# Performance work log

Hardware: AMD Instinct MI355X
Metric: run time of the kernel (lower is better)

The kernel has to match this reference:

```python
import jax, jax.numpy as jnp
import numpy as np

B, DM, L = 16, 512, 1024
D_INNER, D_STATE, D_CONV, DT_RANK = 1024, 16, 4, 32


def setup_inputs() -> dict:
    key = jax.random.key(0)
    ks = jax.random.split(key, 10)
    x = jax.random.normal(ks[0], (B, DM, L), dtype=jnp.float32)
    W_in = jax.random.normal(ks[1], (DM, 2 * D_INNER), dtype=jnp.float32) * 0.02
    conv_w = jax.random.normal(ks[2], (D_INNER, D_CONV), dtype=jnp.float32) * 0.1
    conv_b = jnp.zeros((D_INNER,), dtype=jnp.float32)
    W_x = jax.random.normal(ks[3], (D_INNER, DT_RANK + 2 * D_STATE), dtype=jnp.float32) * 0.02
    W_dt = jax.random.normal(ks[4], (DT_RANK, D_INNER), dtype=jnp.float32) * (DT_RANK ** -0.5)
    dt = jnp.exp(jax.random.uniform(ks[5], (D_INNER,), dtype=jnp.float32)
                 * (np.log(0.1) - np.log(1e-3)) + np.log(1e-3))
    dt_bias = dt + jnp.log(-jnp.expm1(-dt))  # inverse softplus
    A_log = jnp.log(jnp.tile(jnp.arange(1, D_STATE + 1, dtype=jnp.float32)[None, :], (D_INNER, 1)))
    D_skip = jnp.ones((D_INNER,), dtype=jnp.float32)
    W_out = jax.random.normal(ks[6], (D_INNER, DM), dtype=jnp.float32) * 0.02
    gamma = jnp.ones((DM,), dtype=jnp.float32)
    beta = jnp.zeros((DM,), dtype=jnp.float32)
    return {"x": x, "W_in": W_in, "conv_w": conv_w, "conv_b": conv_b, "W_x": W_x,
            "W_dt": W_dt, "dt_bias": dt_bias, "A_log": A_log, "D_skip": D_skip,
            "W_out": W_out, "gamma": gamma, "beta": beta}


def _mamba(xt, W_in, conv_w, conv_b, W_x, W_dt, dt_bias, A_log, D_skip, W_out):
    # xt: [B, L, DM]
    b, l, _ = xt.shape
    xz = xt @ W_in                                   # [B, L, 2*D_INNER]
    xi, z = jnp.split(xz, 2, axis=-1)                # each [B, L, D_INNER]
    # causal depthwise conv1d, kernel D_CONV
    xp = jnp.pad(xi, ((0, 0), (D_CONV - 1, 0), (0, 0)))
    xc = sum(xp[:, k:k + l, :] * conv_w[None, None, :, k] for k in range(D_CONV))
    xc = jax.nn.silu(xc + conv_b)                    # [B, L, D_INNER]
    proj = xc @ W_x                                  # [B, L, DT_RANK + 2*D_STATE]
    dt_in = proj[..., :DT_RANK]
    Bm = proj[..., DT_RANK:DT_RANK + D_STATE]        # [B, L, D_STATE]
    Cm = proj[..., DT_RANK + D_STATE:]               # [B, L, D_STATE]
    delta = jax.nn.softplus(dt_in @ W_dt + dt_bias)  # [B, L, D_INNER]
    A = -jnp.exp(A_log)                              # [D_INNER, D_STATE]

    def step(h, inp):
        d, bt, ct, u = inp                           # [B,Di], [B,Ds], [B,Ds], [B,Di]
        dA = jnp.exp(d[:, :, None] * A[None])        # [B, Di, Ds]
        h = dA * h + d[:, :, None] * bt[:, None, :] * u[:, :, None]
        y = jnp.einsum('bds,bs->bd', h, ct)
        return h, y

    h0 = jnp.zeros((b, D_INNER, D_STATE), dtype=xt.dtype)
    elems = (jnp.swapaxes(delta, 0, 1), jnp.swapaxes(Bm, 0, 1),
             jnp.swapaxes(Cm, 0, 1), jnp.swapaxes(xc, 0, 1))
    _, ys = jax.lax.scan(step, h0, elems)            # ys: [L, B, D_INNER]
    y = jnp.swapaxes(ys, 0, 1) + xc * D_skip
    y = y * jax.nn.silu(z)
    return y @ W_out                                 # [B, L, DM]


def reference(x, W_in, conv_w, conv_b, W_x, W_dt, dt_bias, A_log, D_skip, W_out, gamma, beta):
    xt = jnp.swapaxes(x, 1, 2)                       # (B, DM, L) -> (B, L, DM)
    xt = xt + _mamba(xt, W_in, conv_w, conv_b, W_x, W_dt, dt_bias, A_log, D_skip, W_out)
    mu = jnp.mean(xt, axis=-1, keepdims=True)
    var = jnp.mean(jnp.square(xt - mu), axis=-1, keepdims=True)
    xt = (xt - mu) * jax.lax.rsqrt(var + 1e-5) * gamma + beta
    return jnp.swapaxes(xt, 1, 2)                    # back to (B, DM, L)
```

## Files before the change

kernel.cpp:

```cpp
#include <hip/hip_runtime.h>
#include <hip/hip_bf16.h>
#include <math.h>

#define B_SZ 16
#define DM 512
#define LSEQ 1024
#define DI 1024
#define DSTATE 16
#define DTR 32
#define MROWS (B_SZ * LSEQ)
#define NC 16
#define SCH (LSEQ / NC)
#define PF 4

typedef __attribute__((ext_vector_type(8))) short bf16x8;
typedef __attribute__((ext_vector_type(4))) float f32x4;

__device__ inline float bfu2f(unsigned short u) {
  union { unsigned int i; float f; } c; c.i = ((unsigned int)u) << 16; return c.f;
}
__device__ inline unsigned short f2bfu(float f) {
  union { float f; unsigned int i; } c; c.f = f;
  unsigned int r = c.i + 0x7fff + ((c.i >> 16) & 1);
  return (unsigned short)(r >> 16);
}
__device__ inline f32x4 splat4(float x) { return (f32x4){x, x, x, x}; }

__device__ inline void gl_lds16(const unsigned short* g, unsigned short* l) {
  __builtin_amdgcn_global_load_lds(
      (const __attribute__((address_space(1))) unsigned int*)g,
      (__attribute__((address_space(3))) unsigned int*)l, 16, 0, 0);
}

__global__ void transpose_x_k(const float* __restrict__ x, unsigned short* __restrict__ xtb) {
  __shared__ float t[32][33];
  int b = blockIdx.z;
  int l0 = blockIdx.x * 32, dm0 = blockIdx.y * 32;
  int tx = threadIdx.x, ty = threadIdx.y;
  for (int i = ty; i < 32; i += 8)
    t[i][tx] = x[((long)b * DM + dm0 + i) * LSEQ + l0 + tx];
  __syncthreads();
  for (int i = ty; i < 32; i += 8) {
    long o = ((long)b * LSEQ + l0 + i) * DM + dm0 + tx;
    xtb[o] = f2bfu(t[tx][i]);
  }
}

__global__ void wtrans_k(const float* __restrict__ W, unsigned short* __restrict__ Wt,
                         int N, int K) {
  __shared__ float t[32][33];
  int n0 = blockIdx.x * 32, k0 = blockIdx.y * 32;
  int tx = threadIdx.x, ty = threadIdx.y;
  for (int i = ty; i < 32; i += 8)
    t[i][tx] = W[(long)(k0 + i) * N + n0 + tx];
  __syncthreads();
  for (int i = ty; i < 32; i += 8)
    Wt[(long)(n0 + i) * K + k0 + tx] = f2bfu(t[tx][i]);
}

template <int BM, int BN, int WMN, int WNN, int EPI>
__global__ __launch_bounds__(256, 4) void gemm_bt(
    const unsigned short* __restrict__ A, const unsigned short* __restrict__ Bt,
    void* __restrict__ outp, void* __restrict__ outp2,
    const unsigned short* __restrict__ res, int N, int K) {
  constexpr int WM = BM / WMN;
  constexpr int WN = BN / WNN;
  constexpr int MR = WM / 16;
  constexpr int NR = WN / 16;
  __shared__ __align__(16) unsigned short As[2][BM * 32];
  __shared__ __align__(16) unsigned short Bs[2][BN * 32];
  const int tid = threadIdx.x;
  const int lane = tid & 63;
  const int w = tid >> 6;
  const int wm = w / WNN, wn = w % WNN;
  const long rowT = (long)blockIdx.y * BM;
  const long colT = (long)blockIdx.x * BN;

  f32x4 acc[MR][NR];
#pragma unroll
  for (int m = 0; m < MR; ++m)
#pragma unroll
    for (int n = 0; n < NR; ++n)
      acc[m][n] = (f32x4){0.f, 0.f, 0.f, 0.f};

  const int mrow = wm * WM + (lane & 15);
  const int ncol = wn * WN + (lane & 15);
  const int k8 = (lane >> 4) * 8;
  const int srow = (lane >> 2);
  const int scol = (lane & 3) * 8;

  auto STAGE = [&](int buf, int k0) {
#pragma unroll
    for (int i = 0; i < BM / 64; ++i) {
      int r = i * 64 + w * 16;
      gl_lds16(A + (rowT + r + srow) * K + k0 + scol, &As[buf][r * 32]);
    }
#pragma unroll
    for (int i = 0; i < BN / 64; ++i) {
      int r = i * 64 + w * 16;
      gl_lds16(Bt + (colT + r + srow) * K + k0 + scol, &Bs[buf][r * 32]);
    }
  };

  STAGE(0, 0);
  __syncthreads();
  int cur = 0;
  const int NT = K / 32;
  for (int kt = 0; kt < NT; ++kt) {
    if (kt + 1 < NT) STAGE(cur ^ 1, (kt + 1) * 32);
    bf16x8 af[MR], bfr[NR];
#pragma unroll
    for (int m = 0; m < MR; ++m)
      af[m] = *(const bf16x8*)(&As[cur][(mrow + m * 16) * 32 + k8]);
#pragma unroll
    for (int n = 0; n < NR; ++n)
      bfr[n] = *(const bf16x8*)(&Bs[cur][(ncol + n * 16) * 32 + k8]);
#pragma unroll
    for (int m = 0; m < MR; ++m)
#pragma unroll
      for (int n = 0; n < NR; ++n)
        acc[m][n] = __builtin_amdgcn_mfma_f32_16x16x32_bf16(af[m], bfr[n], acc[m][n], 0, 0, 0);
    __syncthreads();
    cur ^= 1;
  }

  if (EPI == 3) {
    unsigned short* obase = (colT < DI) ? (unsigned short*)outp : (unsigned short*)outp2;
    const long csub = (colT < DI) ? 0 : DI;
#pragma unroll
    for (int m = 0; m < MR; ++m)
#pragma unroll
      for (int n = 0; n < NR; ++n)
#pragma unroll
        for (int r = 0; r < 4; ++r) {
          long row = rowT + wm * WM + m * 16 + (lane >> 4) * 4 + r;
          long col = colT + wn * WN + n * 16 + (lane & 15) - csub;
          obase[row * DI + col] = f2bfu(acc[m][n][r]);
        }
  } else {
#pragma unroll
    for (int m = 0; m < MR; ++m)
#pragma unroll
      for (int n = 0; n < NR; ++n)
#pragma unroll
        for (int r = 0; r < 4; ++r) {
          long row = rowT + wm * WM + m * 16 + (lane >> 4) * 4 + r;
          long col = colT + wn * WN + n * 16 + (lane & 15);
          float v = acc[m][n][r];
          if (EPI == 0)
            ((float*)outp)[row * N + col] = v;
          else
            ((float*)outp)[row * N + col] = v + bfu2f(res[row * N + col]);
        }
  }
}

template <int BM, int BN, int WMN, int WNN, int EPI>
__global__ __launch_bounds__(512, 4) void gemm_bt8(
    const unsigned short* __restrict__ A, const unsigned short* __restrict__ Bt,
    void* __restrict__ outp, void* __restrict__ outp2,
    const unsigned short* __restrict__ res, int N, int K) {
  constexpr int WM = BM / WMN;
  constexpr int WN = BN / WNN;
  constexpr int MR = WM / 16;
  constexpr int NR = WN / 16;
  __shared__ __align__(16) unsigned short As[2][BM * 32];
  __shared__ __align__(16) unsigned short Bs[2][BN * 32];
  const int tid = threadIdx.x;
  const int lane = tid & 63;
  const int w = tid >> 6;
  const int wm = w / WNN, wn = w % WNN;
  const long rowT = (long)blockIdx.y * BM;
  const long colT = (long)blockIdx.x * BN;

  f32x4 acc[MR][NR];
#pragma unroll
  for (int m = 0; m < MR; ++m)
#pragma unroll
    for (int n = 0; n < NR; ++n)
      acc[m][n] = (f32x4){0.f, 0.f, 0.f, 0.f};

  const int mrow = wm * WM + (lane & 15);
  const int ncol = wn * WN + (lane & 15);
  const int k8 = (lane >> 4) * 8;
  const int srow = (lane >> 2);
  const int scol = (lane & 3) * 8;

  auto STAGE = [&](int buf, int k0) {
#pragma unroll
    for (int i = 0; i < BM / 128; ++i) {
      int r = i * 128 + w * 16;
      gl_lds16(A + (rowT + r + srow) * K + k0 + scol, &As[buf][r * 32]);
    }
#pragma unroll
    for (int i = 0; i < BN / 128; ++i) {
      int r = i * 128 + w * 16;
      gl_lds16(Bt + (colT + r + srow) * K + k0 + scol, &Bs[buf][r * 32]);
    }
  };

  STAGE(0, 0);
  __syncthreads();
  int cur = 0;
  const int NT = K / 32;
  for (int kt = 0; kt < NT; ++kt) {
    if (kt + 1 < NT) STAGE(cur ^ 1, (kt + 1) * 32);
    bf16x8 af[MR], bfr[NR];
#pragma unroll
    for (int m = 0; m < MR; ++m)
      af[m] = *(const bf16x8*)(&As[cur][(mrow + m * 16) * 32 + k8]);
#pragma unroll
    for (int n = 0; n < NR; ++n)
      bfr[n] = *(const bf16x8*)(&Bs[cur][(ncol + n * 16) * 32 + k8]);
#pragma unroll
    for (int m = 0; m < MR; ++m)
#pragma unroll
      for (int n = 0; n < NR; ++n)
        acc[m][n] = __builtin_amdgcn_mfma_f32_16x16x32_bf16(af[m], bfr[n], acc[m][n], 0, 0, 0);
    __syncthreads();
    cur ^= 1;
  }

  if (EPI == 3) {
    unsigned short* obase = (colT < DI) ? (unsigned short*)outp : (unsigned short*)outp2;
    const long csub = (colT < DI) ? 0 : DI;
#pragma unroll
    for (int m = 0; m < MR; ++m)
#pragma unroll
      for (int n = 0; n < NR; ++n)
#pragma unroll
        for (int r = 0; r < 4; ++r) {
          long row = rowT + wm * WM + m * 16 + (lane >> 4) * 4 + r;
          long col = colT + wn * WN + n * 16 + (lane & 15) - csub;
          obase[row * DI + col] = f2bfu(acc[m][n][r]);
        }
  } else {
#pragma unroll
    for (int m = 0; m < MR; ++m)
#pragma unroll
      for (int n = 0; n < NR; ++n)
#pragma unroll
        for (int r = 0; r < 4; ++r) {
          long row = rowT + wm * WM + m * 16 + (lane >> 4) * 4 + r;
          long col = colT + wn * WN + n * 16 + (lane & 15);
          float v = acc[m][n][r];
          if (EPI == 0)
            ((float*)outp)[row * N + col] = v;
          else
            ((float*)outp)[row * N + col] = v + bfu2f(res[row * N + col]);
        }
  }
}

__global__ __launch_bounds__(256) void conv_silu_k(
    const unsigned short* __restrict__ xi, const float* __restrict__ conv_w,
    const float* __restrict__ conv_b, unsigned short* __restrict__ xcb) {
  int idx = blockIdx.x * 256 + threadIdx.x;
  int d8 = idx & 127;
  long row = idx >> 7;
  int l = (int)(row & (LSEQ - 1));
  int d0 = d8 * 8;
  float acc[8];
  f32x4 w0[8];
#pragma unroll
  for (int j = 0; j < 8; ++j) {
    acc[j] = conv_b[d0 + j];
    w0[j] = *(const f32x4*)(conv_w + (long)(d0 + j) * 4);
  }
#pragma unroll
  for (int k = 0; k < 4; ++k) {
    int ls = l - 3 + k;
    if (ls < 0) continue;
    uint4 raw = *(const uint4*)(xi + (row - 3 + k) * DI + d0);
    const unsigned short* pv = (const unsigned short*)&raw;
#pragma unroll
    for (int j = 0; j < 8; ++j)
      acc[j] = fmaf(bfu2f(pv[j]), w0[j][k], acc[j]);
  }
  unsigned short o[8];
#pragma unroll
  for (int j = 0; j < 8; ++j) {
    float v = acc[j];
    o[j] = f2bfu(v / (1.f + __expf(-v)));
  }
  *(uint4*)(xcb + row * DI + d0) = *(uint4*)o;
}

__global__ __launch_bounds__(256) void delta_k(
    const float* __restrict__ proj, const float* __restrict__ W_dt,
    const float* __restrict__ dt_bias, unsigned short* __restrict__ delta) {
  __shared__ float wlds[DTR][256];
  const int tid = threadIdx.x;
  const int d0 = blockIdx.x * 256;
  const int d = d0 + tid;
#pragma unroll
  for (int k = 0; k < DTR; ++k)
    wlds[k][tid] = W_dt[(long)k * DI + d0 + tid];
  __syncthreads();
  const float bias = dt_bias[d];
  const long r0 = (long)blockIdx.y * 16;
  const float* pp = proj + r0 * 64;
  float acc[16];
#pragma unroll
  for (int r = 0; r < 16; ++r) acc[r] = bias;
#pragma unroll
  for (int k = 0; k < DTR; ++k) {
    float w = wlds[k][tid];
#pragma unroll
    for (int r = 0; r < 16; ++r)
      acc[r] = fmaf(pp[r * 64 + k], w, acc[r]);
  }
#pragma unroll
  for (int r = 0; r < 16; ++r) {
    float a = acc[r];
    float sp = a > 20.f ? a : __logf(1.f + __expf(a));
    delta[(r0 + r) * DI + d] = f2bfu(sp);
  }
}

__global__ __launch_bounds__(256) void scan_p1(
    const unsigned short* __restrict__ delta, const unsigned short* __restrict__ xcb,
    const float* __restrict__ proj, const float* __restrict__ A_log,
    float* __restrict__ Hbuf, float* __restrict__ sdbuf) {
  __shared__ __align__(16) f32x4 bs[SCH][4];
  const int tid = threadIdx.x;
  const int b = blockIdx.z;
  const int c = blockIdx.y;
  const int d = blockIdx.x * 256 + tid;
  const long rowbase = (long)b * LSEQ + (long)c * SCH;

  {
    int r = tid >> 2, q = tid & 3;
    bs[r][q] = *(const f32x4*)(proj + (rowbase + r) * 64 + 32 + q * 4);
  }
  __syncthreads();

  const float* Ap = A_log + (long)d * DSTATE;
  bool fast = true;
#pragma unroll
  for (int j = 0; j < DSTATE; ++j)
    fast = fast && (fabsf(__expf(Ap[j]) - (float)(j + 1)) < 1e-3f);

  f32x4 h[4];
#pragma unroll
  for (int j = 0; j < 4; ++j) h[j] = (f32x4){0.f, 0.f, 0.f, 0.f};
  float sumdv = 0.f;
  const unsigned short* dp = delta + rowbase * DI + d;
  const unsigned short* up = xcb + rowbase * DI + d;

  if (fast) {
    float dvb[PF], ub[PF];
#pragma unroll
    for (int j = 0; j < PF; ++j) {
      dvb[j] = bfu2f(dp[j * DI]);
      ub[j] = bfu2f(up[j * DI]);
    }
    for (int g = 0; g < SCH; g += PF) {
      float dvn[PF], un[PF];
#pragma unroll
      for (int j = 0; j < PF; ++j) {
        dvn[j] = bfu2f(dp[(g + PF + j) * DI]);
        un[j] = bfu2f(up[(g + PF + j) * DI]);
      }
#pragma unroll
      for (int j = 0; j < PF; ++j) {
        float dv = dvb[j], u = ub[j];
        sumdv += dv;
        float du = dv * u;
        float q = __expf(-dv);
        float q2 = q * q, q3 = q2 * q, q4 = q2 * q2;
        float q8 = q4 * q4, q12 = q8 * q4;
        f32x4 qv = (f32x4){q, q2, q3, q4};
        f32x4 du4 = splat4(du);
        h[0] = qv * h[0] + du4 * bs[g + j][0];
        h[1] = splat4(q4) * qv * h[1] + du4 * bs[g + j][1];
        h[2] = splat4(q8) * qv * h[2] + du4 * bs[g + j][2];
        h[3] = splat4(q12) * qv * h[3] + du4 * bs[g + j][3];
      }
#pragma unroll
      for (int j = 0; j < PF; ++j) { dvb[j] = dvn[j]; ub[j] = un[j]; }
    }
  } else {
    float A[16];
#pragma unroll
    for (int j = 0; j < DSTATE; ++j) A[j] = -__expf(Ap[j]);
    for (int li = 0; li < SCH; ++li) {
      float dv = bfu2f(dp[li * DI]);
      float u = bfu2f(up[li * DI]);
      sumdv += dv;
      float du = dv * u;
#pragma unroll
      for (int j = 0; j < 4; ++j) {
        f32x4 bv = bs[li][j];
        f32x4 pv = (f32x4){__expf(dv * A[4 * j]), __expf(dv * A[4 * j + 1]),
                           __expf(dv * A[4 * j + 2]), __expf(dv * A[4 * j + 3])};
        h[j] = pv * h[j] + splat4(du) * bv;
      }
    }
  }
  long hoff = (((long)b * NC + c) * DI + d) * DSTATE;
#pragma unroll
  for (int j = 0; j < 4; ++j) *(f32x4*)(Hbuf + hoff + 4 * j) = h[j];
  sdbuf[((long)b * NC + c) * DI + d] = sumdv;
}

__global__ __launch_bounds__(256) void scan_p2(
    const float* __restrict__ A_log, const float* __restrict__ sdbuf,
    float* __restrict__ Hbuf) {
  const int tid = threadIdx.x;
  const int s = tid & 15;
  const int d = blockIdx.x * 16 + (tid >> 4);
  const int b = blockIdx.y;
  const float A = -__expf(A_log[(long)d * DSTATE + s]);
  float hrun = 0.f;
#pragma unroll
  for (int c = 0; c < NC; ++c) {
    long off = (((long)b * NC + c) * DI + d) * DSTATE + s;
    float Hloc = Hbuf[off];
    float sd = sdbuf[((long)b * NC + c) * DI + d];
    Hbuf[off] = hrun;
    hrun = __expf(A * sd) * hrun + Hloc;
  }
}

__global__ __launch_bounds__(256) void scan_p3(
    const unsigned short* __restrict__ delta, const unsigned short* __restrict__ xcb,
    const unsigned short* __restrict__ zb, const float* __restrict__ proj,
    const float* __restrict__ A_log, const float* __restrict__ D_skip,
    const float* __restrict__ Hbuf, unsigned short* __restrict__ yb) {
  __shared__ __align__(16) f32x4 bs[SCH][8];
  const int tid = threadIdx.x;
  const int b = blockIdx.z;
  const int c = blockIdx.y;
  const int d = blockIdx.x * 256 + tid;
  const long rowbase = (long)b * LSEQ + (long)c * SCH;

#pragma unroll
  for (int k = 0; k < 2; ++k) {
    int i = tid + k * 256;
    int r = i >> 3, q = i & 7;
    bs[r][q] = *(const f32x4*)(proj + (rowbase + r) * 64 + 32 + q * 4);
  }
  __syncthreads();

  const float* Ap = A_log + (long)d * DSTATE;
  bool fast = true;
#pragma unroll
  for (int j = 0; j < DSTATE; ++j)
    fast = fast && (fabsf(__expf(Ap[j]) - (float)(j + 1)) < 1e-3f);

  long hoff = (((long)b * NC + c) * DI + d) * DSTATE;
  f32x4 h[4];
#pragma unroll
  for (int j = 0; j < 4; ++j) h[j] = *(const f32x4*)(Hbuf + hoff + 4 * j);
  const float Dsk = D_skip[d];

  const unsigned short* dp = delta + rowbase * DI + d;
  const unsigned short* up = xcb + rowbase * DI + d;
  const unsigned short* zp = zb + rowbase * DI + d;
  unsigned short* yp = yb + rowbase * DI + d;

  if (fast) {
    float dvb[PF], ub[PF], zvb[PF];
#pragma unroll
    for (int j = 0; j < PF; ++j) {
      dvb[j] = bfu2f(dp[j * DI]);
      ub[j] = bfu2f(up[j * DI]);
      zvb[j] = bfu2f(zp[j * DI]);
    }
    for (int g = 0; g < SCH; g += PF) {
      float dvn[PF], un[PF], zvn[PF];
#pragma unroll
      for (int j = 0; j < PF; ++j) {
        dvn[j] = bfu2f(dp[(g + PF + j) * DI]);
        un[j] = bfu2f(up[(g + PF + j) * DI]);
        zvn[j] = bfu2f(zp[(g + PF + j) * DI]);
      }
#pragma unroll
      for (int j = 0; j < PF; ++j) {
        float dv = dvb[j], u = ub[j], zv = zvb[j];
        float du = dv * u;
        float q = __expf(-dv);
        float q2 = q * q, q3 = q2 * q, q4 = q2 * q2;
        float q8 = q4 * q4, q12 = q8 * q4;
        f32x4 qv = (f32x4){q, q2, q3, q4};
        f32x4 du4 = splat4(du);
        h[0] = qv * h[0] + du4 * bs[g + j][0];
        h[1] = splat4(q4) * qv * h[1] + du4 * bs[g + j][1];
        h[2] = splat4(q8) * qv * h[2] + du4 * bs[g + j][2];
        h[3] = splat4(q12) * qv * h[3] + du4 * bs[g + j][3];
        f32x4 yv = h[0] * bs[g + j][4] + h[1] * bs[g + j][5];
        yv = yv + h[2] * bs[g + j][6] + h[3] * bs[g + j][7];
        float y = (yv[0] + yv[1]) + (yv[2] + yv[3]);
        float yg = (y + u * Dsk) * (zv / (1.f + __expf(-zv)));
        yp[(g + j) * DI] = f2bfu(yg);
      }
#pragma unroll
      for (int j = 0; j < PF; ++j) { dvb[j] = dvn[j]; ub[j] = un[j]; zvb[j] = zvn[j]; }
    }
  } else {
    float A[16];
#pragma unroll
    for (int j = 0; j < DSTATE; ++j) A[j] = -__expf(Ap[j]);
    for (int li = 0; li < SCH; ++li) {
      float dv = bfu2f(dp[li * DI]);
      float u = bfu2f(up[li * DI]);
      float zv = bfu2f(zp[li * DI]);
      float du = dv * u;
      f32x4 yv = (f32x4){0.f, 0.f, 0.f, 0.f};
#pragma unroll
      for (int j = 0; j < 4; ++j) {
        f32x4 pv = (f32x4){__expf(dv * A[4 * j]), __expf(dv * A[4 * j + 1]),
                           __expf(dv * A[4 * j + 2]), __expf(dv * A[4 * j + 3])};
        h[j] = pv * h[j] + splat4(du) * bs[li][j];
        yv = yv + h[j] * bs[li][4 + j];
      }
      float y = (yv[0] + yv[1]) + (yv[2] + yv[3]);
      float yg = (y + u * Dsk) * (zv / (1.f + __expf(-zv)));
      yp[li * DI] = f2bfu(yg);
    }
  }
}

__global__ __launch_bounds__(64) void ln_stats_k(const float* __restrict__ p,
                                                 float* __restrict__ mu,
                                                 float* __restrict__ rs) {
  long row = blockIdx.x;
  int lane = threadIdx.x;
  const float* pr = p + row * DM + lane * 8;
  f32x4 a = *(const f32x4*)pr;
  f32x4 c = *(const f32x4*)(pr + 4);
  float s = a[0] + a[1] + a[2] + a[3] + c[0] + c[1] + c[2] + c[3];
  float ss = a[0] * a[0] + a[1] * a[1] + a[2] * a[2] + a[3] * a[3] +
             c[0] * c[0] + c[1] * c[1] + c[2] * c[2] + c[3] * c[3];
#pragma unroll
  for (int off = 32; off >= 1; off >>= 1) {
    s += __shfl_xor(s, off);
    ss += __shfl_xor(ss, off);
  }
  if (lane == 0) {
    float m = s * (1.f / DM);
    float v = ss * (1.f / DM) - m * m;
    mu[row] = m;
    rs[row] = rsqrtf(v + 1e-5f);
  }
}

__global__ void ln_apply_k(const float* __restrict__ pre, const float* __restrict__ mu,
                           const float* __restrict__ rs, const float* __restrict__ gamma,
                           const float* __restrict__ beta, float* __restrict__ out) {
  __shared__ float t[32][33];
  int b = blockIdx.z;
  int l0 = blockIdx.x * 32, dm0 = blockIdx.y * 32;
  int tx = threadIdx.x, ty = threadIdx.y;
  for (int i = ty; i < 32; i += 8) {
    long row = (long)b * LSEQ + l0 + i;
    float v = pre[row * DM + dm0 + tx];
    t[i][tx] = (v - mu[row]) * rs[row] * gamma[dm0 + tx] + beta[dm0 + tx];
  }
  __syncthreads();
  for (int i = ty; i < 32; i += 8)
    out[((long)b * DM + dm0 + i) * LSEQ + l0 + tx] = t[tx][i];
}

extern "C" void kernel_launch(void* const* d_in, const int* in_sizes, int n_in,
                              void* d_out, int out_size, void* d_ws, size_t ws_size,
                              hipStream_t stream) {
  const float* x = (const float*)d_in[0];
  const float* W_in = (const float*)d_in[1];
  const float* conv_w = (const float*)d_in[2];
  const float* conv_b = (const float*)d_in[3];
  const float* W_x = (const float*)d_in[4];
  const float* W_dt = (const float*)d_in[5];
  const float* dt_bias = (const float*)d_in[6];
  const float* A_log = (const float*)d_in[7];
  const float* D_skip = (const float*)d_in[8];
  const float* W_out = (const float*)d_in[9];
  const float* gamma = (const float*)d_in[10];
  const float* beta = (const float*)d_in[11];
  float* out = (float*)d_out;

  char* p = (char*)d_ws;
  auto alloc = [&](size_t bytes) {
    char* r = p;
    p += (bytes + 255) & ~(size_t)255;
    return r;
  };
  unsigned short* xtb = (unsigned short*)alloc((size_t)MROWS * DM * 2);
  unsigned short* xib = (unsigned short*)alloc((size_t)MROWS * DI * 2);
  unsigned short* zb  = (unsigned short*)alloc((size_t)MROWS * DI * 2);
  unsigned short* xcb = (unsigned short*)alloc((size_t)MROWS * DI * 2);
  float* proj = (float*)alloc((size_t)MROWS * 64 * 4);
  unsigned short* dbuf = (unsigned short*)alloc((size_t)MROWS * DI * 2);
  float* sdbuf = (float*)alloc((size_t)B_SZ * NC * DI * 4);
  unsigned short* WinT = (unsigned short*)alloc((size_t)2 * DI * DM * 2);
  unsigned short* WxT = (unsigned short*)alloc((size_t)64 * DI * 2);
  unsigned short* WoutT = (unsigned short*)alloc((size_t)DM * DI * 2);
  float* mu = (float*)alloc((size_t)MROWS * 4);
  float* rs = (float*)alloc((size_t)MROWS * 4);
  unsigned short* yb = xib;
  float* preLN = (float*)dbuf;
  float* Hbuf = out;

  transpose_x_k<<<dim3(LSEQ / 32, DM / 32, B_SZ), dim3(32, 8), 0, stream>>>(x, xtb);
  wtrans_k<<<dim3(2 * DI / 32, DM / 32), dim3(32, 8), 0, stream>>>(W_in, WinT, 2 * DI, DM);
  wtrans_k<<<dim3(64 / 32, DI / 32), dim3(32, 8), 0, stream>>>(W_x, WxT, 64, DI);
  wtrans_k<<<dim3(DM / 32, DI / 32), dim3(32, 8), 0, stream>>>(W_out, WoutT, DM, DI);

  gemm_bt8<256, 128, 4, 2, 3><<<dim3(2 * DI / 128, MROWS / 256), 512, 0, stream>>>(
      xtb, WinT, xib, zb, nullptr, 2 * DI, DM);
  conv_silu_k<<<(MROWS * 128) / 256, 256, 0, stream>>>(xib, conv_w, conv_b, xcb);
  gemm_bt<64, 64, 4, 1, 0><<<dim3(1, MROWS / 64), 256, 0, stream>>>(
      xcb, WxT, proj, nullptr, nullptr, 64, DI);
  delta_k<<<dim3(DI / 256, MROWS / 16), 256, 0, stream>>>(proj, W_dt, dt_bias, dbuf);
  scan_p1<<<dim3(DI / 256, NC, B_SZ), 256, 0, stream>>>(dbuf, xcb, proj, A_log, Hbuf, sdbuf);
  scan_p2<<<dim3(DI / 16, B_SZ), 256, 0, stream>>>(A_log, sdbuf, Hbuf);
  scan_p3<<<dim3(DI / 256, NC, B_SZ), 256, 0, stream>>>(dbuf, xcb, zb, proj, A_log, D_skip,
                                                        Hbuf, yb);
  gemm_bt<128, 128, 2, 2, 2><<<dim3(DM / 128, MROWS / 128), 256, 0, stream>>>(
      yb, WoutT, preLN, nullptr, xtb, DM, DI);
  ln_stats_k<<<MROWS, 64, 0, stream>>>(preLN, mu, rs);
  ln_apply_k<<<dim3(LSEQ / 32, DM / 32, B_SZ), dim3(32, 8), 0, stream>>>(
      preLN, mu, rs, gamma, beta, out);
}
```

Measured before the change: 302.1 us.

## Store pre-LayerNorm residual in bf16 and fuse LN stats with apply-transpose

The output GEMM epilogue now writes the residual sum as bf16 instead of fp32, halving the intermediate buffer's traffic. The separate LayerNorm statistics and apply/transpose kernels are replaced by one kernel that loads 32 rows, reduces mean and variance with 8-lane shuffles, normalizes, and writes the transposed output through shared memory in two halves. This removes one launch and a full re-read of the intermediate, at the cost of rounding the pre-LN values to bf16 and a large shared tile with heavy register use per thread.

```diff
diff --git a/kernel.cpp b/kernel.cpp
--- a/kernel.cpp
+++ b/kernel.cpp
@@ -150,7 +150,8 @@
           if (EPI == 0)
             ((float*)outp)[row * N + col] = v;
           else
-            ((float*)outp)[row * N + col] = v + bfu2f(res[row * N + col]);
+            ((unsigned short*)outp)[row * N + col] =
+                f2bfu(v + bfu2f(res[row * N + col]));
         }
   }
 }
@@ -247,7 +248,8 @@
           if (EPI == 0)
             ((float*)outp)[row * N + col] = v;
           else
-            ((float*)outp)[row * N + col] = v + bfu2f(res[row * N + col]);
+            ((unsigned short*)outp)[row * N + col] =
+                f2bfu(v + bfu2f(res[row * N + col]));
         }
   }
 }
@@ -522,45 +524,58 @@
   }
 }
 
-__global__ __launch_bounds__(64) void ln_stats_k(const float* __restrict__ p,
-                                                 float* __restrict__ mu,
-                                                 float* __restrict__ rs) {
-  long row = blockIdx.x;
-  int lane = threadIdx.x;
-  const float* pr = p + row * DM + lane * 8;
-  f32x4 a = *(const f32x4*)pr;
-  f32x4 c = *(const f32x4*)(pr + 4);
-  float s = a[0] + a[1] + a[2] + a[3] + c[0] + c[1] + c[2] + c[3];
-  float ss = a[0] * a[0] + a[1] * a[1] + a[2] * a[2] + a[3] * a[3] +
-             c[0] * c[0] + c[1] * c[1] + c[2] * c[2] + c[3] * c[3];
-#pragma unroll
-  for (int off = 32; off >= 1; off >>= 1) {
+__global__ __launch_bounds__(256) void ln_fused_k(
+    const unsigned short* __restrict__ pre, const float* __restrict__ gamma,
+    const float* __restrict__ beta, float* __restrict__ out) {
+  __shared__ float t[32][257];
+  const int tid = threadIdx.x;
+  const int b = blockIdx.y;
+  const int l0 = blockIdx.x * 32;
+  const int r = tid >> 3;
+  const int c0 = (tid & 7) * 64;
+  const long row = (long)b * LSEQ + l0 + r;
+
+  unsigned short vals[64];
+#pragma unroll
+  for (int k = 0; k < 8; ++k)
+    *(uint4*)(vals + k * 8) = *(const uint4*)(pre + row * DM + c0 + k * 8);
+
+  float f[64];
+  float s = 0.f, ss = 0.f;
+#pragma unroll
+  for (int i = 0; i < 64; ++i) {
+    float v = bfu2f(vals[i]);
+    f[i] = v;
+    s += v;
+    ss += v * v;
+  }
+#pragma unroll
+  for (int off = 1; off < 8; off <<= 1) {
     s += __shfl_xor(s, off);
     ss += __shfl_xor(ss, off);
   }
-  if (lane == 0) {
-    float m = s * (1.f / DM);
-    float v = ss * (1.f / DM) - m * m;
-    mu[row] = m;
-    rs[row] = rsqrtf(v + 1e-5f);
-  }
-}
-
-__global__ void ln_apply_k(const float* __restrict__ pre, const float* __restrict__ mu,
-                           const float* __restrict__ rs, const float* __restrict__ gamma,
-                           const float* __restrict__ beta, float* __restrict__ out) {
-  __shared__ float t[32][33];
-  int b = blockIdx.z;
-  int l0 = blockIdx.x * 32, dm0 = blockIdx.y * 32;
-  int tx = threadIdx.x, ty = threadIdx.y;
-  for (int i = ty; i < 32; i += 8) {
-    long row = (long)b * LSEQ + l0 + i;
-    float v = pre[row * DM + dm0 + tx];
-    t[i][tx] = (v - mu[row]) * rs[row] * gamma[dm0 + tx] + beta[dm0 + tx];
-  }
-  __syncthreads();
-  for (int i = ty; i < 32; i += 8)
-    out[((long)b * DM + dm0 + i) * LSEQ + l0 + tx] = t[tx][i];
+  const float m = s * (1.f / DM);
+  const float rstd = rsqrtf(ss * (1.f / DM) - m * m + 1e-5f);
+
+#pragma unroll
+  for (int i = 0; i < 64; ++i)
+    f[i] = (f[i] - m) * rstd * gamma[c0 + i] + beta[c0 + i];
+
+#pragma unroll
+  for (int half = 0; half < 2; ++half) {
+    __syncthreads();
+    if ((c0 >> 8) == half) {
+      int cb = c0 - half * 256;
+#pragma unroll
+      for (int i = 0; i < 64; ++i) t[r][cb + i] = f[i];
+    }
+    __syncthreads();
+    const int tx = tid & 31;
+    for (int i = tid >> 5; i < 256; i += 8) {
+      long dm = half * 256 + i;
+      out[((long)b * DM + dm) * LSEQ + l0 + tx] = t[tx][i];
+    }
+  }
 }
 
 extern "C" void kernel_launch(void* const* d_in, const int* in_sizes, int n_in,
@@ -596,10 +611,8 @@
   unsigned short* WinT = (unsigned short*)alloc((size_t)2 * DI * DM * 2);
   unsigned short* WxT = (unsigned short*)alloc((size_t)64 * DI * 2);
   unsigned short* WoutT = (unsigned short*)alloc((size_t)DM * DI * 2);
-  float* mu = (float*)alloc((size_t)MROWS * 4);
-  float* rs = (float*)alloc((size_t)MROWS * 4);
   unsigned short* yb = xib;
-  float* preLN = (float*)dbuf;
+  unsigned short* preLNb = dbuf;
   float* Hbuf = out;
 
   transpose_x_k<<<dim3(LSEQ / 32, DM / 32, B_SZ), dim3(32, 8), 0, stream>>>(x, xtb);
@@ -618,8 +631,6 @@
   scan_p3<<<dim3(DI / 256, NC, B_SZ), 256, 0, stream>>>(dbuf, xcb, zb, proj, A_log, D_skip,
                                                         Hbuf, yb);
   gemm_bt<128, 128, 2, 2, 2><<<dim3(DM / 128, MROWS / 128), 256, 0, stream>>>(
-      yb, WoutT, preLN, nullptr, xtb, DM, DI);
-  ln_stats_k<<<MROWS, 64, 0, stream>>>(preLN, mu, rs);
-  ln_apply_k<<<dim3(LSEQ / 32, DM / 32, B_SZ), dim3(32, 8), 0, stream>>>(
-      preLN, mu, rs, gamma, beta, out);
-}
+      yb, WoutT, preLNb, nullptr, xtb, DM, DI);
+  ln_fused_k<<<dim3(LSEQ / 32, B_SZ), 256, 0, stream>>>(preLNb, gamma, beta, out);
+}
```

Result: no change. 300.4 us, median of 2 (-0.5%).
